# Kernel optimization log

Measured on AMD Instinct MI355X. Metric: run time of the kernel, lower is better.

The kernel has to match this reference:

```python
import jax, jax.numpy as jnp
import numpy as np

D_MODEL = 1024
D_INNER = 1024          # expand=1
NQK = 32
NV = 32
DSTATE = 64
DCONV = 4
CHUNK = 128
CONV_DIM = D_INNER + 2 * NQK * DSTATE          # 5120
HEADDIM = D_INNER // NV                         # 32
IN_PROJ_OUT = 2 * D_INNER + 2 * NQK * DSTATE + NV  # 6176


def setup_inputs() -> dict:
    key = jax.random.key(0)
    ks = jax.random.split(key, 6)
    B, L = 2, 8192
    u = jax.random.normal(ks[0], (B, L, D_MODEL), jnp.float32)
    W_in = jax.random.normal(ks[1], (IN_PROJ_OUT, D_MODEL), jnp.float32) * 0.02
    conv_w = jax.random.normal(ks[2], (CONV_DIM, DCONV), jnp.float32) * 0.2
    conv_b = jax.random.normal(ks[3], (CONV_DIM,), jnp.float32) * 0.02
    z_bias = jnp.zeros((D_INNER,), jnp.float32)
    D = jnp.ones((NV,), jnp.float32)
    W_out = jax.random.normal(ks[4], (D_MODEL, D_INNER), jnp.float32) * 0.02
    return {"u": u, "W_in": W_in, "conv_w": conv_w, "conv_b": conv_b,
            "z_bias": z_bias, "D": D, "W_out": W_out}


def _segsum(x):
    # x: (b,h,c,l) -> (b,h,c,l,l); entry (i,j) = sum_{j<s<=i} x_s for i>=j, masked else
    l = x.shape[-1]
    cs = jnp.cumsum(x, -1)
    seg = cs[..., :, None] - cs[..., None, :]
    mask = jnp.tril(jnp.ones((l, l), bool))
    return jnp.where(mask, seg, -1e9)


def reference(u, W_in, conv_w, conv_b, z_bias, D, W_out):
    b, L, _ = u.shape
    # in_proj and split: xBC | z | A_log
    xBCzA = u @ W_in.T
    xBC = xBCzA[..., :CONV_DIM]
    z = xBCzA[..., CONV_DIM:CONV_DIM + D_INNER]
    A_log = xBCzA[..., CONV_DIM + D_INNER:]          # (b,L,NV)
    # causal depthwise conv1d, identity activation
    xp = jnp.pad(xBC, ((0, 0), (DCONV - 1, 0), (0, 0)))
    xBC = sum(conv_w[:, k] * xp[:, k:k + L, :] for k in range(DCONV)) + conv_b
    # split x, B, C and reshape to heads
    x = xBC[..., :D_INNER].reshape(b, L, NV, HEADDIM)
    Bm = xBC[..., D_INNER:D_INNER + NQK * DSTATE].reshape(b, L, NQK, DSTATE)
    Cm = xBC[..., D_INNER + NQK * DSTATE:].reshape(b, L, NQK, DSTATE)
    # dt = softplus(A_log); A = -1 per head; kernel uses (x/dt) and multiplies dt back in
    dt = jax.nn.softplus(A_log)                      # (b,L,h)
    x_sc = x / dt[..., None]
    Xdt = x_sc * dt[..., None]
    Adt = -dt
    # chunked SSD (mamba_chunk_scan_combined math)
    nc = L // CHUNK
    Ac = Adt.reshape(b, nc, CHUNK, NV).transpose(0, 3, 1, 2)   # (b,h,c,l)
    A_cum = jnp.cumsum(Ac, -1)
    Lmat = jnp.exp(_segsum(Ac))                                # (b,h,c,l,l)
    Bc = Bm.reshape(b, nc, CHUNK, NQK, DSTATE)
    Cc = Cm.reshape(b, nc, CHUNK, NQK, DSTATE)
    Xc = Xdt.reshape(b, nc, CHUNK, NV, HEADDIM)
    # intra-chunk (diagonal block) output
    Y_diag = jnp.einsum('bclhn,bcshn,bhcls,bcshp->bclhp', Cc, Bc, Lmat, Xc)
    # per-chunk final states
    decay_states = jnp.exp(A_cum[..., -1:] - A_cum)            # (b,h,c,l)
    states = jnp.einsum('bclhn,bhcl,bclhp->bchpn', Bc, decay_states, Xc)
    dc = jnp.exp(A_cum[..., -1])                               # (b,h,c)
    st = jnp.moveaxis(states, 1, 0)                            # (c,b,h,p,n)
    dcs = jnp.moveaxis(dc, 2, 0)                               # (c,b,h)

    def step(S, inp):
        s_c, d_c = inp
        prev = S
        S = S * d_c[..., None, None] + s_c
        return S, prev

    S0 = jnp.zeros((b, NV, HEADDIM, DSTATE), Xdt.dtype)
    _, prevs = jax.lax.scan(step, S0, (st, dcs))               # (c,b,h,p,n)
    prevs = jnp.moveaxis(prevs, 0, 1)                          # (b,c,h,p,n)
    # inter-chunk (off-diagonal) contribution
    Y_off = jnp.einsum('bclhn,bchpn,bhcl->bclhp', Cc, prevs, jnp.exp(A_cum))
    y = (Y_diag + Y_off).reshape(b, L, NV, HEADDIM)
    # skip connection uses the UNscaled x (per torch code)
    y = y + D[None, None, :, None] * x
    y = y.reshape(b, L, D_INNER)
    # gated output projection
    return (y * jax.nn.silu(z + z_bias)) @ W_out.T
```

## Files before the change

### kernel.cpp

```cpp
#include <hip/hip_runtime.h>

typedef unsigned short u16;
typedef unsigned int   u32;
typedef __bf16  bf16x8 __attribute__((ext_vector_type(8)));
typedef float   f32x4  __attribute__((ext_vector_type(4)));
typedef unsigned int u32x4 __attribute__((ext_vector_type(4)));
typedef unsigned int u32x2 __attribute__((ext_vector_type(2)));

__device__ __forceinline__ float bf2f(u16 h){ return __uint_as_float(((u32)h)<<16); }
__device__ __forceinline__ u16 f2bf(float f){
  u32 u = __float_as_uint(f);
  u += 0x7FFFu + ((u>>16)&1u);
  return (u16)(u>>16);
}
__device__ __forceinline__ f32x4 mfma16(bf16x8 a, bf16x8 b, f32x4 c){
  return __builtin_amdgcn_mfma_f32_16x16x32_bf16(a,b,c,0,0,0);
}
__device__ __forceinline__ void ld16_lds(const u16* g, u16* l){
  __builtin_amdgcn_global_load_lds((const __attribute__((address_space(1))) u32*)g,
                                   (__attribute__((address_space(3))) u32*)l, 16, 0, 0);
}

__global__ __launch_bounds__(256) void cvt_kernel(const float* __restrict__ in,
                                                  u16* __restrict__ out, int n4){
  int i = blockIdx.x*256 + threadIdx.x;
  if (i < n4){
    float4 v = ((const float4*)in)[i];
    u32 p0 = (u32)f2bf(v.x) | ((u32)f2bf(v.y)<<16);
    u32 p1 = (u32)f2bf(v.z) | ((u32)f2bf(v.w)<<16);
    u32x2 pv = {p0, p1};
    *(u32x2*)(out + (size_t)i*4) = pv;
  }
}

__global__ __launch_bounds__(256) void dt_kernel(const float* __restrict__ u,
                                                 const float* __restrict__ Win,
                                                 float* __restrict__ dtb){
  __shared__ float us[8][1028];
  const int tid = threadIdx.x;
  const size_t t0 = (size_t)blockIdx.x*8;
  for (int i=tid; i<2048; i+=256){
    int row = i>>8, col = (i&255)*4;
    *(float4*)&us[row][col] = *(const float4*)(u + (t0+row)*1024 + col);
  }
  __syncthreads();
  const int tok = tid & 7, h = tid >> 3;
  const float* wp = Win + (size_t)(6144+h)*1024;
  float s0=0.f,s1=0.f,s2=0.f,s3=0.f;
  for (int k=0;k<1024;k+=4){
    float4 a  = *(const float4*)&us[tok][k];
    float4 wv = *(const float4*)&wp[k];
    s0 += a.x*wv.x; s1 += a.y*wv.y; s2 += a.z*wv.z; s3 += a.w*wv.w;
  }
  float s = (s0+s1)+(s2+s3);
  dtb[(t0+tok)*32 + h] = (s > 15.f) ? s : log1pf(expf(s));
}

__global__ __launch_bounds__(256,2) void gemm_in(const u16* __restrict__ A,
                                                 const u16* __restrict__ Bw,
                                                 u16* __restrict__ out0,
                                                 u16* __restrict__ out1,
                                                 const float* __restrict__ zb){
  __shared__ u16 As[128*32];
  __shared__ u16 Bs[128*32];
  const int tid  = threadIdx.x;
  const int lane = tid & 63;
  const int w = tid >> 6, wm = w >> 1, wn = w & 1;
  const int quad = lane >> 4, l15 = lane & 15;
  const size_t m0 = (size_t)blockIdx.y*128, n0 = (size_t)blockIdx.x*128;

  f32x4 acc[4][4];
  #pragma unroll
  for (int i=0;i<4;i++)
    #pragma unroll
    for (int j=0;j<4;j++){ f32x4 z = {0.f,0.f,0.f,0.f}; acc[i][j] = z; }

  const int srow = w*16 + (lane>>2);
  const int scol = (lane&3)*8;
  const u16* gA = A  + (m0+srow)*1024 + scol;
  const u16* gB = Bw + (n0+srow)*1024 + scol;
  u16* lA = As + w*512;
  u16* lB = Bs + w*512;

  for (int k0 = 0; k0 < 1024; k0 += 32){
    __syncthreads();
    ld16_lds(gA,          lA);
    ld16_lds(gA + 64*1024, lA + 2048);
    ld16_lds(gB,          lB);
    ld16_lds(gB + 64*1024, lB + 2048);
    gA += 32; gB += 32;
    __syncthreads();
    bf16x8 av[4], bv[4];
    #pragma unroll
    for (int mi=0;mi<4;mi++) av[mi] = *(const bf16x8*)&As[(wm*64+mi*16+l15)*32 + quad*8];
    #pragma unroll
    for (int ni=0;ni<4;ni++) bv[ni] = *(const bf16x8*)&Bs[(wn*64+ni*16+l15)*32 + quad*8];
    #pragma unroll
    for (int mi=0;mi<4;mi++)
      #pragma unroll
      for (int ni=0;ni<4;ni++)
        acc[mi][ni] = mfma16(av[mi], bv[ni], acc[mi][ni]);
  }

  #pragma unroll
  for (int mi=0;mi<4;mi++){
    #pragma unroll
    for (int ni=0;ni<4;ni++){
      #pragma unroll
      for (int r=0;r<4;r++){
        size_t row = m0 + wm*64 + mi*16 + quad*4 + r;
        int    col = (int)n0 + wn*64 + ni*16 + l15;
        float v = acc[mi][ni][r];
        if (col < 5120){
          out0[row*5120 + col] = f2bf(v);
        } else {
          int ch = col - 5120;
          float z = v + zb[ch];
          float sg = z / (1.f + __expf(-z));
          out1[row*1024 + ch] = f2bf(sg);
        }
      }
    }
  }
}

__global__ __launch_bounds__(256,2) void gemm_out(const u16* __restrict__ A,
                                                  const u16* __restrict__ Bw,
                                                  float* __restrict__ out0){
  __shared__ u16 As[128*32];
  __shared__ u16 Bs[128*32];
  const int tid  = threadIdx.x;
  const int lane = tid & 63;
  const int w = tid >> 6, wm = w >> 1, wn = w & 1;
  const int quad = lane >> 4, l15 = lane & 15;
  const size_t m0 = (size_t)blockIdx.y*128, n0 = (size_t)blockIdx.x*128;

  f32x4 acc[4][4];
  #pragma unroll
  for (int i=0;i<4;i++)
    #pragma unroll
    for (int j=0;j<4;j++){ f32x4 z = {0.f,0.f,0.f,0.f}; acc[i][j] = z; }

  const int srow = w*16 + (lane>>2);
  const int scol = (lane&3)*8;
  const u16* gA = A  + (m0+srow)*1024 + scol;
  const u16* gB = Bw + (n0+srow)*1024 + scol;
  u16* lA = As + w*512;
  u16* lB = Bs + w*512;

  for (int k0 = 0; k0 < 1024; k0 += 32){
    __syncthreads();
    ld16_lds(gA,          lA);
    ld16_lds(gA + 64*1024, lA + 2048);
    ld16_lds(gB,          lB);
    ld16_lds(gB + 64*1024, lB + 2048);
    gA += 32; gB += 32;
    __syncthreads();
    bf16x8 av[4], bv[4];
    #pragma unroll
    for (int mi=0;mi<4;mi++) av[mi] = *(const bf16x8*)&As[(wm*64+mi*16+l15)*32 + quad*8];
    #pragma unroll
    for (int ni=0;ni<4;ni++) bv[ni] = *(const bf16x8*)&Bs[(wn*64+ni*16+l15)*32 + quad*8];
    #pragma unroll
    for (int mi=0;mi<4;mi++)
      #pragma unroll
      for (int ni=0;ni<4;ni++)
        acc[mi][ni] = mfma16(av[mi], bv[ni], acc[mi][ni]);
  }

  #pragma unroll
  for (int mi=0;mi<4;mi++)
    #pragma unroll
    for (int ni=0;ni<4;ni++)
      #pragma unroll
      for (int r=0;r<4;r++){
        size_t row = m0 + wm*64 + mi*16 + quad*4 + r;
        int    col = (int)n0 + wn*64 + ni*16 + l15;
        out0[row*1024 + col] = acc[mi][ni][r];
      }
}

__global__ __launch_bounds__(256) void conv_kernel(const u16* __restrict__ xraw,
                                                   const float* __restrict__ cw,
                                                   const float* __restrict__ cb,
                                                   u16* __restrict__ xconv){
  const int c  = blockIdx.x*256 + threadIdx.x;
  const int t0 = blockIdx.y*8;
  const float w0=cw[c*4+0], w1=cw[c*4+1], w2=cw[c*4+2], w3=cw[c*4+3], bias=cb[c];
  const size_t base = (size_t)c;
  float h0 = (t0>=3) ? bf2f(xraw[base + (size_t)(t0-3)*5120]) : 0.f;
  float h1 = (t0>=2) ? bf2f(xraw[base + (size_t)(t0-2)*5120]) : 0.f;
  float h2 = (t0>=1) ? bf2f(xraw[base + (size_t)(t0-1)*5120]) : 0.f;
  #pragma unroll
  for (int i=0;i<8;i++){
    float x = bf2f(xraw[base + (size_t)(t0+i)*5120]);
    float o = w0*h0 + w1*h1 + w2*h2 + w3*x + bias;
    xconv[base + (size_t)(t0+i)*5120] = f2bf(o);
    h0=h1; h1=h2; h2=x;
  }
}

__global__ __launch_bounds__(256,1) void chunk1_kernel(const u16* __restrict__ xconv,
                                                       const float* __restrict__ dtb,
                                                       const float* __restrict__ Dvec,
                                                       float* __restrict__ ypart,
                                                       float* __restrict__ states,
                                                       float* __restrict__ dcb){
  __shared__ u16 Ps[128*136];
  __shared__ u16 XT[32*136];
  __shared__ u16 BT[64*136];
  __shared__ float Acum[128];
  __shared__ float decay[128];

  const int tid = threadIdx.x;
  const int lane = tid & 63;
  const int w = tid >> 6, quad = lane >> 4, l15 = lane & 15;
  const int blk = blockIdx.x;
  const int h = blk & 31, c = blk >> 5;
  const size_t tok0 = (size_t)c*128;
  const size_t xbase = tok0 * 5120;

  float mdt = 0.f;
  if (tid < 128) mdt = -dtb[(tok0 + tid)*32 + h];

  #pragma unroll
  for (int p=0;p<2;p++){
    int idx = p*256 + tid;
    int row = idx >> 2, col = (idx & 3)*8;
    u32x4 v = *(const u32x4*)(xconv + xbase + (size_t)row*5120 + h*32 + col);
    const u16* pv = (const u16*)&v;
    #pragma unroll
    for (int j=0;j<8;j++) XT[(col+j)*136 + row] = pv[j];
  }
  #pragma unroll
  for (int p=0;p<4;p++){
    int idx = p*256 + tid;
    int row = idx >> 3, col = (idx & 7)*8;
    u32x4 v = *(const u32x4*)(xconv + xbase + (size_t)row*5120 + 1024 + h*64 + col);
    const u16* pv = (const u16*)&v;
    #pragma unroll
    for (int j=0;j<8;j++) BT[(col+j)*136 + row] = pv[j];
  }
  if (tid < 128) Acum[tid] = mdt;
  __syncthreads();
  float run = mdt;
  for (int off=1; off<128; off<<=1){
    float add = 0.f;
    if (tid < 128 && tid >= off) add = Acum[tid-off];
    __syncthreads();
    if (tid < 128){ run += add; Acum[tid] = run; }
    __syncthreads();
  }
  float Alast = Acum[127];
  if (tid < 128) decay[tid] = __expf(Alast - Acum[tid]);
  if (tid == 0)  dcb[blk] = __expf(Alast);

  const int wm = w >> 1, wn = w & 1;
  f32x4 g[4][4];
  #pragma unroll
  for (int i=0;i<4;i++)
    #pragma unroll
    for (int j=0;j<4;j++){ f32x4 z = {0.f,0.f,0.f,0.f}; g[i][j] = z; }
  #pragma unroll
  for (int kk=0; kk<2; kk++){
    bf16x8 av[4], bv[4];
    #pragma unroll
    for (int mi=0;mi<4;mi++){
      int row = wm*64 + mi*16 + l15;
      av[mi] = *(const bf16x8*)(xconv + xbase + (size_t)row*5120 + 3072 + h*64 + kk*32 + quad*8);
    }
    #pragma unroll
    for (int ni=0;ni<4;ni++){
      int row = wn*64 + ni*16 + l15;
      bv[ni] = *(const bf16x8*)(xconv + xbase + (size_t)row*5120 + 1024 + h*64 + kk*32 + quad*8);
    }
    #pragma unroll
    for (int mi=0;mi<4;mi++)
      #pragma unroll
      for (int ni=0;ni<4;ni++)
        g[mi][ni] = mfma16(av[mi], bv[ni], g[mi][ni]);
  }
  #pragma unroll
  for (int mi=0;mi<4;mi++){
    int rowb = wm*64 + mi*16 + quad*4;
    #pragma unroll
    for (int ni=0;ni<4;ni++){
      int col = wn*64 + ni*16 + l15;
      float ac = Acum[col];
      #pragma unroll
      for (int r=0;r<4;r++){
        int row = rowb + r;
        float val = 0.f;
        if (col <= row) val = g[mi][ni][r] * __expf(Acum[row] - ac);
        Ps[row*136 + col] = f2bf(val);
      }
    }
  }
  __syncthreads();

  f32x4 yd[2][2];
  #pragma unroll
  for (int i=0;i<2;i++)
    #pragma unroll
    for (int j=0;j<2;j++){ f32x4 z = {0.f,0.f,0.f,0.f}; yd[i][j] = z; }
  #pragma unroll
  for (int kk=0;kk<4;kk++){
    bf16x8 av[2], bv[2];
    #pragma unroll
    for (int mi=0;mi<2;mi++) av[mi] = *(const bf16x8*)&Ps[(w*32+mi*16+l15)*136 + kk*32 + quad*8];
    #pragma unroll
    for (int ni=0;ni<2;ni++) bv[ni] = *(const bf16x8*)&XT[(ni*16+l15)*136 + kk*32 + quad*8];
    #pragma unroll
    for (int mi=0;mi<2;mi++)
      #pragma unroll
      for (int ni=0;ni<2;ni++)
        yd[mi][ni] = mfma16(av[mi], bv[ni], yd[mi][ni]);
  }
  float Dh = Dvec[h];
  #pragma unroll
  for (int mi=0;mi<2;mi++)
    #pragma unroll
    for (int ni=0;ni<2;ni++)
      #pragma unroll
      for (int r=0;r<4;r++){
        int row = w*32 + mi*16 + quad*4 + r;
        int col = ni*16 + l15;
        float xval = bf2f(XT[col*136 + row]);
        ypart[(tok0+row)*1024 + h*32 + col] = yd[mi][ni][r] + Dh*xval;
      }

  const int wm2 = w >> 1, wn2 = w & 1;
  f32x4 st[2];
  { f32x4 z = {0.f,0.f,0.f,0.f}; st[0]=z; st[1]=z; }
  #pragma unroll
  for (int kk=0;kk<4;kk++){
    bf16x8 av;
    {
      u32x4 xv = *(const u32x4*)&XT[(wm2*16+l15)*136 + kk*32 + quad*8];
      const u16* xp = (const u16*)&xv;
      #pragma unroll
      for (int j=0;j<8;j++) ((__bf16*)&av)[j] = (__bf16)(bf2f(xp[j]) * decay[kk*32 + quad*8 + j]);
    }
    bf16x8 bv[2];
    #pragma unroll
    for (int ni=0;ni<2;ni++) bv[ni] = *(const bf16x8*)&BT[(wn2*32+ni*16+l15)*136 + kk*32 + quad*8];
    #pragma unroll
    for (int ni=0;ni<2;ni++) st[ni] = mfma16(av, bv[ni], st[ni]);
  }
  size_t sbase = (size_t)blk * 2048;
  #pragma unroll
  for (int ni=0;ni<2;ni++)
    #pragma unroll
    for (int r=0;r<4;r++){
      int row = wm2*16 + quad*4 + r;
      int col = wn2*32 + ni*16 + l15;
      states[sbase + row*64 + col] = st[ni][r];
    }
}

__global__ __launch_bounds__(256) void scan_kernel(float* __restrict__ states,
                                                   const float* __restrict__ dcb){
  const int h = blockIdx.x >> 3;
  const int part = blockIdx.x & 7;
  const int pn = part*256 + threadIdx.x;
  float S = 0.f;
  for (int c=0;c<64;c++){
    size_t idx = ((size_t)(c*32 + h))*2048 + pn;
    float stv = states[idx];
    float d = dcb[c*32 + h];
    states[idx] = S;
    S = S*d + stv;
  }
}

__global__ __launch_bounds__(256,1) void chunk3_kernel(const u16* __restrict__ xconv,
                                                       const float* __restrict__ dtb,
                                                       const float* __restrict__ prevs,
                                                       const float* __restrict__ ypart,
                                                       const u16* __restrict__ gate,
                                                       u16* __restrict__ yg){
  __shared__ u16 Pv[32*72];
  __shared__ float Acum[128];
  const int tid = threadIdx.x;
  const int lane = tid & 63;
  const int w = tid >> 6, quad = lane >> 4, l15 = lane & 15;
  const int blk = blockIdx.x;
  const int h = blk & 31, c = blk >> 5;
  const size_t tok0 = (size_t)c*128;
  const size_t xbase = tok0 * 5120;

  float mdt = 0.f;
  if (tid < 128) mdt = -dtb[(tok0 + tid)*32 + h];
  size_t sbase = (size_t)blk * 2048;
  #pragma unroll
  for (int p=0;p<8;p++){
    int i = p*256 + tid;
    int pp = i >> 6, nn = i & 63;
    Pv[pp*72 + nn] = f2bf(prevs[sbase + i]);
  }
  if (tid < 128) Acum[tid] = mdt;
  __syncthreads();
  float run = mdt;
  for (int off=1; off<128; off<<=1){
    float add = 0.f;
    if (tid < 128 && tid >= off) add = Acum[tid-off];
    __syncthreads();
    if (tid < 128){ run += add; Acum[tid] = run; }
    __syncthreads();
  }

  f32x4 yo[2][2];
  #pragma unroll
  for (int i=0;i<2;i++)
    #pragma unroll
    for (int j=0;j<2;j++){ f32x4 z = {0.f,0.f,0.f,0.f}; yo[i][j] = z; }
  #pragma unroll
  for (int kk=0;kk<2;kk++){
    bf16x8 av[2], bv[2];
    #pragma unroll
    for (int mi=0;mi<2;mi++){
      int row = w*32 + mi*16 + l15;
      av[mi] = *(const bf16x8*)(xconv + xbase + (size_t)row*5120 + 3072 + h*64 + kk*32 + quad*8);
    }
    #pragma unroll
    for (int ni=0;ni<2;ni++) bv[ni] = *(const bf16x8*)&Pv[(ni*16+l15)*72 + kk*32 + quad*8];
    #pragma unroll
    for (int mi=0;mi<2;mi++)
      #pragma unroll
      for (int ni=0;ni<2;ni++)
        yo[mi][ni] = mfma16(av[mi], bv[ni], yo[mi][ni]);
  }
  #pragma unroll
  for (int mi=0;mi<2;mi++)
    #pragma unroll
    for (int ni=0;ni<2;ni++)
      #pragma unroll
      for (int r=0;r<4;r++){
        int row = w*32 + mi*16 + quad*4 + r;
        int col = ni*16 + l15;
        size_t gi = (tok0+row)*1024 + h*32 + col;
        float val = (ypart[gi] + __expf(Acum[row]) * yo[mi][ni][r]) * bf2f(gate[gi]);
        yg[gi] = f2bf(val);
      }
}

extern "C" void kernel_launch(void* const* d_in, const int* in_sizes, int n_in,
                              void* d_out, int out_size, void* d_ws, size_t ws_size,
                              hipStream_t stream){
  (void)out_size; (void)ws_size;
  static const int want[7] = {16777216, 6324224, 20480, 5120, 1024, 32, 1048576};
  const void* src[7] = {nullptr,nullptr,nullptr,nullptr,nullptr,nullptr,nullptr};
  if (n_in >= 7){
    for (int i=0;i<7;i++)
      for (int j=0;j<n_in;j++)
        if (in_sizes[j] == want[i]){ src[i] = d_in[j]; break; }
  }
  bool ok = true;
  for (int i=0;i<7;i++) if (!src[i]) ok = false;
  if (!ok) for (int i=0;i<7;i++) src[i] = d_in[i];
  const float* u      = (const float*)src[0];
  const float* W_in   = (const float*)src[1];
  const float* conv_w = (const float*)src[2];
  const float* conv_b = (const float*)src[3];
  const float* z_bias = (const float*)src[4];
  const float* Dvec   = (const float*)src[5];
  const float* W_out  = (const float*)src[6];
  float* out = (float*)d_out;

  char* p = (char*)d_ws;
  u16* wi_bf   = (u16*)p;   p += (size_t)6144*1024*2;
  u16* wo_bf   = (u16*)p;   p += (size_t)1024*1024*2;
  u16* u_bf    = (u16*)p;   p += (size_t)16384*1024*2;
  float* dtb   = (float*)p; p += (size_t)16384*32*4;
  float* dcb   = (float*)p; p += (size_t)4096*4;
  u16* gate    = (u16*)p;   p += (size_t)8192*1024*2;
  u16* yg      = (u16*)p;   p += (size_t)8192*1024*2;
  char* xbcA   = p;         p += (size_t)8192*5120*2;
  u16* xconv   = (u16*)p;   p += (size_t)8192*5120*2;

  u16*   xbc_raw = (u16*)xbcA;
  float* ypart   = (float*)xbcA;
  float* states  = (float*)(xbcA + (size_t)8192*1024*4);

  cvt_kernel<<<16384, 256, 0, stream>>>(u,     u_bf,  16384*1024/4);
  cvt_kernel<<<6144,  256, 0, stream>>>(W_in,  wi_bf, 6144*1024/4);
  cvt_kernel<<<1024,  256, 0, stream>>>(W_out, wo_bf, 1024*1024/4);
  dt_kernel<<<2048, 256, 0, stream>>>(u, W_in, dtb);

  for (int b = 0; b < 2; b++){
    const u16* ub_bf = u_bf + (size_t)b*8192*1024;
    float*     dtb_b = dtb  + (size_t)b*8192*32;
    float*     dcb_b = dcb  + (size_t)b*2048;
    float*     out_b = out  + (size_t)b*8192*1024;
    gemm_in<<<dim3(48,64), 256, 0, stream>>>(ub_bf, wi_bf, xbc_raw, gate, z_bias);
    conv_kernel<<<dim3(20,1024), 256, 0, stream>>>(xbc_raw, conv_w, conv_b, xconv);
    chunk1_kernel<<<2048, 256, 0, stream>>>(xconv, dtb_b, Dvec, ypart, states, dcb_b);
    scan_kernel<<<256, 256, 0, stream>>>(states, dcb_b);
    chunk3_kernel<<<2048, 256, 0, stream>>>(xconv, dtb_b, states, ypart, gate, yg);
    gemm_out<<<dim3(8,64), 256, 0, stream>>>(yg, wo_bf, out_b);
  }
}
```

Before: 798.5 us.

## Replace input-projection GEMM with 256x256 double-buffered swizzled MFMA kernel

The 128x128 input-projection GEMM is replaced by a 512-thread kernel that computes 256x256 tiles with a BK=64 double-buffered LDS pipeline. Global-to-LDS loads for the next tile are issued inside each compute phase and gated with explicit vmcnt waits and raw barriers. The LDS layout is XOR-swizzled to avoid bank conflicts, and s_setprio is raised around the MFMA blocks. The aim is more data reuse per tile and hiding load latency behind compute. The cost is 128KB of LDS and one block per CU, which lowers occupancy and makes the hand-written barrier sequencing fragile.

```diff
diff --git a/kernel.cpp b/kernel.cpp
--- a/kernel.cpp
+++ b/kernel.cpp
@@ -56,62 +56,108 @@
   dtb[(t0+tok)*32 + h] = (s > 15.f) ? s : log1pf(expf(s));
 }
 
-__global__ __launch_bounds__(256,2) void gemm_in(const u16* __restrict__ A,
-                                                 const u16* __restrict__ Bw,
-                                                 u16* __restrict__ out0,
-                                                 u16* __restrict__ out1,
-                                                 const float* __restrict__ zb){
-  __shared__ u16 As[128*32];
-  __shared__ u16 Bs[128*32];
+#define VMC4 asm volatile("s_waitcnt vmcnt(4)" ::: "memory")
+#define VMC0 asm volatile("s_waitcnt vmcnt(0)" ::: "memory")
+
+#define STAGE_A(DB,KH,KT) do{ \
+  ld16_lds(gA0 + (KT)*64 + (KH)*32, Asm + (DB)*16384 + (KH)*8192        + w*512); \
+  ld16_lds(gA1 + (KT)*64 + (KH)*32, Asm + (DB)*16384 + (KH)*8192 + 4096 + w*512); }while(0)
+#define STAGE_B(DB,KH,KT) do{ \
+  ld16_lds(gB0 + (KT)*64 + (KH)*32, Bsm + (DB)*16384 + (KH)*8192        + w*512); \
+  ld16_lds(gB1 + (KT)*64 + (KH)*32, Bsm + (DB)*16384 + (KH)*8192 + 4096 + w*512); }while(0)
+
+#define PHASE(DB, KH, MQ, LOADB, STAGE_STMT, VM_STMT)                                   \
+  {                                                                                     \
+    bf16x8 av[4];                                                                       \
+    _Pragma("unroll")                                                                   \
+    for (int mi=0; mi<4; mi++)                                                          \
+      av[mi] = *(const bf16x8*)&Asm[(DB)*16384 + (KH)*8192 + (MQ)*2048 + mi*512 + aoff];\
+    if (LOADB){                                                                         \
+      _Pragma("unroll")                                                                 \
+      for (int ni=0; ni<4; ni++)                                                        \
+        bv[ni] = *(const bf16x8*)&Bsm[(DB)*16384 + (KH)*8192 + ni*512 + boff];          \
+    }                                                                                   \
+    STAGE_STMT;                                                                         \
+    __builtin_amdgcn_s_barrier();                                                       \
+    __builtin_amdgcn_s_setprio(1);                                                      \
+    _Pragma("unroll")                                                                   \
+    for (int mi=0; mi<4; mi++)                                                          \
+      _Pragma("unroll")                                                                 \
+      for (int ni=0; ni<4; ni++)                                                        \
+        acc[(MQ)*4+mi][ni] = mfma16(av[mi], bv[ni], acc[(MQ)*4+mi][ni]);                \
+    __builtin_amdgcn_s_setprio(0);                                                      \
+    VM_STMT;                                                                            \
+    __builtin_amdgcn_s_barrier();                                                       \
+  }
+
+#define TILE_MAIN(DB, KT1)                                 \
+  PHASE(DB,0,0,1, STAGE_A(1-(DB),0,(KT1)), ((void)0))      \
+  PHASE(DB,0,1,0, STAGE_B(1-(DB),0,(KT1)), VMC4)           \
+  PHASE(DB,1,0,1, STAGE_A(1-(DB),1,(KT1)), ((void)0))      \
+  PHASE(DB,1,1,0, STAGE_B(1-(DB),1,(KT1)), VMC4)
+
+__global__ __launch_bounds__(512,1) void gemm_in256(const u16* __restrict__ A,
+                                                    const u16* __restrict__ Bw,
+                                                    u16* __restrict__ out0,
+                                                    u16* __restrict__ out1,
+                                                    const float* __restrict__ zb){
+  __shared__ u16 smem[65536];
+  u16* Asm = smem;
+  u16* Bsm = smem + 32768;
+
   const int tid  = threadIdx.x;
   const int lane = tid & 63;
-  const int w = tid >> 6, wm = w >> 1, wn = w & 1;
+  const int w    = tid >> 6;
+  const int wm   = w >> 2;
+  const int wn   = w & 3;
   const int quad = lane >> 4, l15 = lane & 15;
-  const size_t m0 = (size_t)blockIdx.y*128, n0 = (size_t)blockIdx.x*128;
-
-  f32x4 acc[4][4];
-  #pragma unroll
-  for (int i=0;i<4;i++)
+  const size_t m0 = (size_t)blockIdx.y*256, n0 = (size_t)blockIdx.x*256;
+
+  const int srow    = w*16 + (lane>>2);
+  const int scol_sw = ((lane&3) ^ ((lane>>2)&3))*8;
+  const u16* gA0 = A  + (m0 + srow      )*1024 + scol_sw;
+  const u16* gA1 = A  + (m0 + srow + 128)*1024 + scol_sw;
+  const u16* gB0 = Bw + (n0 + srow      )*1024 + scol_sw;
+  const u16* gB1 = Bw + (n0 + srow + 128)*1024 + scol_sw;
+
+  const int swz  = (quad*8) ^ ((l15&3)<<3);
+  const int aoff = (wm*128 + l15)*32 + swz;
+  const int boff = (wn*64  + l15)*32 + swz;
+
+  f32x4 acc[8][4];
+  #pragma unroll
+  for (int i=0;i<8;i++)
     #pragma unroll
     for (int j=0;j<4;j++){ f32x4 z = {0.f,0.f,0.f,0.f}; acc[i][j] = z; }
 
-  const int srow = w*16 + (lane>>2);
-  const int scol = (lane&3)*8;
-  const u16* gA = A  + (m0+srow)*1024 + scol;
-  const u16* gB = Bw + (n0+srow)*1024 + scol;
-  u16* lA = As + w*512;
-  u16* lB = Bs + w*512;
-
-  for (int k0 = 0; k0 < 1024; k0 += 32){
-    __syncthreads();
-    ld16_lds(gA,          lA);
-    ld16_lds(gA + 64*1024, lA + 2048);
-    ld16_lds(gB,          lB);
-    ld16_lds(gB + 64*1024, lB + 2048);
-    gA += 32; gB += 32;
-    __syncthreads();
-    bf16x8 av[4], bv[4];
-    #pragma unroll
-    for (int mi=0;mi<4;mi++) av[mi] = *(const bf16x8*)&As[(wm*64+mi*16+l15)*32 + quad*8];
-    #pragma unroll
-    for (int ni=0;ni<4;ni++) bv[ni] = *(const bf16x8*)&Bs[(wn*64+ni*16+l15)*32 + quad*8];
-    #pragma unroll
-    for (int mi=0;mi<4;mi++)
-      #pragma unroll
-      for (int ni=0;ni<4;ni++)
-        acc[mi][ni] = mfma16(av[mi], bv[ni], acc[mi][ni]);
-  }
-
-  #pragma unroll
-  for (int mi=0;mi<4;mi++){
-    #pragma unroll
-    for (int ni=0;ni<4;ni++){
+  STAGE_A(0,0,0); STAGE_B(0,0,0);
+  STAGE_A(0,1,0); STAGE_B(0,1,0);
+  VMC4;
+  __builtin_amdgcn_s_barrier();
+
+  bf16x8 bv[4];
+  #pragma unroll 1
+  for (int t=0; t<14; t+=2){
+    TILE_MAIN(0, t+1)
+    TILE_MAIN(1, t+2)
+  }
+  TILE_MAIN(0, 15)
+  PHASE(1,0,0,1, ((void)0), ((void)0))
+  PHASE(1,0,1,0, ((void)0), VMC0)
+  PHASE(1,1,0,1, ((void)0), ((void)0))
+  PHASE(1,1,1,0, ((void)0), ((void)0))
+
+  const bool is_z = (n0 >= 5120);
+  #pragma unroll
+  for (int mf=0; mf<8; mf++){
+    #pragma unroll
+    for (int nf=0; nf<4; nf++){
       #pragma unroll
       for (int r=0;r<4;r++){
-        size_t row = m0 + wm*64 + mi*16 + quad*4 + r;
-        int    col = (int)n0 + wn*64 + ni*16 + l15;
-        float v = acc[mi][ni][r];
-        if (col < 5120){
+        size_t row = m0 + wm*128 + mf*16 + quad*4 + r;
+        int    col = (int)n0 + wn*64 + nf*16 + l15;
+        float v = acc[mf][nf][r];
+        if (!is_z){
           out0[row*5120 + col] = f2bf(v);
         } else {
           int ch = col - 5120;
@@ -492,7 +538,7 @@
     float*     dtb_b = dtb  + (size_t)b*8192*32;
     float*     dcb_b = dcb  + (size_t)b*2048;
     float*     out_b = out  + (size_t)b*8192*1024;
-    gemm_in<<<dim3(48,64), 256, 0, stream>>>(ub_bf, wi_bf, xbc_raw, gate, z_bias);
+    gemm_in256<<<dim3(24,32), 512, 0, stream>>>(ub_bf, wi_bf, xbc_raw, gate, z_bias);
     conv_kernel<<<dim3(20,1024), 256, 0, stream>>>(xbc_raw, conv_w, conv_b, xconv);
     chunk1_kernel<<<2048, 256, 0, stream>>>(xconv, dtb_b, Dvec, ypart, states, dcb_b);
     scan_kernel<<<256, 256, 0, stream>>>(states, dcb_b);
```

New measurement: 829.0 us. 1.04x slower.

## Remap GEMM block order for L2 locality, swizzle LDS, preload scan states

Applied to the files above, without the earlier changes.

Both GEMMs now remap the hardware block index so that consecutive blocks are spread across XCD-sized groups, and they XOR-swizzle the LDS column layout on both the global-to-LDS load and the fragment read to cut bank conflicts. The scan kernel loads all 64 chunk states into registers before running the serial recurrence, so the loads are no longer serialized behind the dependency chain. The remap hardcodes grid dimensions (48x? and 8x?) and the scan adds register pressure.

```diff
diff --git a/kernel.cpp b/kernel.cpp
--- a/kernel.cpp
+++ b/kernel.cpp
@@ -67,7 +67,10 @@
   const int lane = tid & 63;
   const int w = tid >> 6, wm = w >> 1, wn = w & 1;
   const int quad = lane >> 4, l15 = lane & 15;
-  const size_t m0 = (size_t)blockIdx.y*128, n0 = (size_t)blockIdx.x*128;
+
+  const int hwid = (int)(blockIdx.y*48 + blockIdx.x);
+  const int tile = (hwid & 7)*384 + (hwid >> 3);
+  const size_t m0 = (size_t)(tile / 48)*128, n0 = (size_t)(tile % 48)*128;
 
   f32x4 acc[4][4];
   #pragma unroll
@@ -75,12 +78,14 @@
     #pragma unroll
     for (int j=0;j<4;j++){ f32x4 z = {0.f,0.f,0.f,0.f}; acc[i][j] = z; }
 
-  const int srow = w*16 + (lane>>2);
-  const int scol = (lane&3)*8;
-  const u16* gA = A  + (m0+srow)*1024 + scol;
-  const u16* gB = Bw + (n0+srow)*1024 + scol;
+  const int srow    = w*16 + (lane>>2);
+  const int scol_sw = ((lane&3) ^ ((lane>>3)&3))*8;
+  const u16* gA = A  + (m0+srow)*1024 + scol_sw;
+  const u16* gB = Bw + (n0+srow)*1024 + scol_sw;
   u16* lA = As + w*512;
   u16* lB = Bs + w*512;
+
+  const int swz = (quad*8) ^ (((l15>>1)&3)<<3);
 
   for (int k0 = 0; k0 < 1024; k0 += 32){
     __syncthreads();
@@ -92,9 +97,9 @@
     __syncthreads();
     bf16x8 av[4], bv[4];
     #pragma unroll
-    for (int mi=0;mi<4;mi++) av[mi] = *(const bf16x8*)&As[(wm*64+mi*16+l15)*32 + quad*8];
-    #pragma unroll
-    for (int ni=0;ni<4;ni++) bv[ni] = *(const bf16x8*)&Bs[(wn*64+ni*16+l15)*32 + quad*8];
+    for (int mi=0;mi<4;mi++) av[mi] = *(const bf16x8*)&As[(wm*64+mi*16+l15)*32 + swz];
+    #pragma unroll
+    for (int ni=0;ni<4;ni++) bv[ni] = *(const bf16x8*)&Bs[(wn*64+ni*16+l15)*32 + swz];
     #pragma unroll
     for (int mi=0;mi<4;mi++)
       #pragma unroll
@@ -133,7 +138,10 @@
   const int lane = tid & 63;
   const int w = tid >> 6, wm = w >> 1, wn = w & 1;
   const int quad = lane >> 4, l15 = lane & 15;
-  const size_t m0 = (size_t)blockIdx.y*128, n0 = (size_t)blockIdx.x*128;
+
+  const int hwid = (int)(blockIdx.y*8 + blockIdx.x);
+  const int tile = (hwid & 7)*64 + (hwid >> 3);
+  const size_t m0 = (size_t)(tile / 8)*128, n0 = (size_t)(tile % 8)*128;
 
   f32x4 acc[4][4];
   #pragma unroll
@@ -141,12 +149,14 @@
     #pragma unroll
     for (int j=0;j<4;j++){ f32x4 z = {0.f,0.f,0.f,0.f}; acc[i][j] = z; }
 
-  const int srow = w*16 + (lane>>2);
-  const int scol = (lane&3)*8;
-  const u16* gA = A  + (m0+srow)*1024 + scol;
-  const u16* gB = Bw + (n0+srow)*1024 + scol;
+  const int srow    = w*16 + (lane>>2);
+  const int scol_sw = ((lane&3) ^ ((lane>>3)&3))*8;
+  const u16* gA = A  + (m0+srow)*1024 + scol_sw;
+  const u16* gB = Bw + (n0+srow)*1024 + scol_sw;
   u16* lA = As + w*512;
   u16* lB = Bs + w*512;
+
+  const int swz = (quad*8) ^ (((l15>>1)&3)<<3);
 
   for (int k0 = 0; k0 < 1024; k0 += 32){
     __syncthreads();
@@ -158,9 +168,9 @@
     __syncthreads();
     bf16x8 av[4], bv[4];
     #pragma unroll
-    for (int mi=0;mi<4;mi++) av[mi] = *(const bf16x8*)&As[(wm*64+mi*16+l15)*32 + quad*8];
-    #pragma unroll
-    for (int ni=0;ni<4;ni++) bv[ni] = *(const bf16x8*)&Bs[(wn*64+ni*16+l15)*32 + quad*8];
+    for (int mi=0;mi<4;mi++) av[mi] = *(const bf16x8*)&As[(wm*64+mi*16+l15)*32 + swz];
+    #pragma unroll
+    for (int ni=0;ni<4;ni++) bv[ni] = *(const bf16x8*)&Bs[(wn*64+ni*16+l15)*32 + swz];
     #pragma unroll
     for (int mi=0;mi<4;mi++)
       #pragma unroll
@@ -363,13 +373,15 @@
   const int h = blockIdx.x >> 3;
   const int part = blockIdx.x & 7;
   const int pn = part*256 + threadIdx.x;
+  float r[64];
+  #pragma unroll
+  for (int c=0;c<64;c++) r[c] = states[((size_t)(c*32 + h))*2048 + pn];
   float S = 0.f;
+  #pragma unroll
   for (int c=0;c<64;c++){
-    size_t idx = ((size_t)(c*32 + h))*2048 + pn;
-    float stv = states[idx];
-    float d = dcb[c*32 + h];
-    states[idx] = S;
-    S = S*d + stv;
+    float stv = r[c];
+    states[((size_t)(c*32 + h))*2048 + pn] = S;
+    S = S*dcb[c*32 + h] + stv;
   }
 }
 
```

Result: no change. 807.6 us (+1.1%).
